# Performance work log

Hardware: AMD Instinct MI355X
Metric: run time of the kernel (lower is better)

The kernel has to match this reference:

```python
import jax, jax.numpy as jnp
import numpy as np

IMG = 224          # image_size
FMAP = (56, 56)    # feature_map_dims (AdaptiveAvgPool2d((56,56)))
K_REWEIGHT = 3     # self.n_reweight
BLUR_RADIUS = 4    # KNNGaussianBlur(4): kernel 9, sigma 4


def _cdist(a, b):
    # Euclidean pairwise distance, [Na, D] x [Nb, D] -> [Na, Nb]
    a2 = jnp.sum(a * a, axis=1, keepdims=True)            # [Na,1]
    b2 = jnp.sum(b * b, axis=1, keepdims=True).T          # [1,Nb]
    d2 = a2 + b2 - 2.0 * (a @ b.T)
    return jnp.sqrt(jnp.maximum(d2, 0.0))


def _gaussian_blur(x):
    # x: [1,1,H,W]; torchvision GaussianBlur(kernel=9, sigma=4), reflect pad
    r, sigma = BLUR_RADIUS, float(BLUR_RADIUS)
    t = jnp.arange(2 * r + 1, dtype=x.dtype) - r
    g = jnp.exp(-(t * t) / (2.0 * sigma * sigma))
    g = g / jnp.sum(g)
    k2d = jnp.outer(g, g)[None, None]                     # [1,1,9,9]
    xp = jnp.pad(x, ((0, 0), (0, 0), (r, r), (r, r)), mode='reflect')
    return jax.lax.conv_general_dilated(
        xp, k2d, window_strides=(1, 1), padding='VALID',
        dimension_numbers=('NCHW', 'OIHW', 'NCHW'))


def setup_inputs() -> dict:
    key = jax.random.key(0)
    k1, k2 = jax.random.split(key)
    patch = jax.random.normal(k1, (FMAP[0] * FMAP[1], 768), dtype=jnp.float32)
    patch_lib = jax.random.normal(k2, (16384, 768), dtype=jnp.float32)
    mean = jnp.zeros((), dtype=jnp.float32)
    std = jnp.ones((), dtype=jnp.float32)
    return {"patch": patch, "patch_lib": patch_lib, "mean": mean, "std": std}


def reference(patch, patch_lib, mean, std):
    # normalization (method_name != 'Point_MAE' branch)
    p = (patch - mean) / std                               # [N, D]

    dist = _cdist(p, patch_lib)                            # [N, Nlib]
    min_val = jnp.min(dist, axis=1)                        # [N]
    min_idx = jnp.argmin(dist, axis=1)                     # [N]
    s_idx = jnp.argmax(min_val)
    s_star = jnp.max(min_val)

    m_test = p[s_idx]                                      # [D]
    m_star = patch_lib[min_idx[s_idx]]                     # [D]

    # distances of m_star to whole bank, k smallest
    w_dist = jnp.sqrt(jnp.maximum(
        jnp.sum((patch_lib - m_star) ** 2, axis=1), 0.0))  # [Nlib]
    _, nn_idx = jax.lax.top_k(-w_dist, K_REWEIGHT)         # smallest k
    m_star_knn = jnp.linalg.norm(
        m_test[None, :] - patch_lib[nn_idx[1:]], axis=1)   # [k-1]

    D_sqrt = jnp.sqrt(jnp.asarray(patch.shape[1], dtype=p.dtype))
    w = 1.0 - jnp.exp(s_star / D_sqrt) / jnp.sum(jnp.exp(m_star_knn / D_sqrt))
    s = w * s_star

    s_map = min_val.reshape(1, 1, *FMAP)
    s_map = jax.image.resize(s_map, (1, 1, IMG, IMG), method='bilinear')
    s_map = _gaussian_blur(s_map)
    return s, s_map
```

## Files before the change

### kernel.cpp

```cpp
#include <hip/hip_runtime.h>
#include <hip/hip_bf16.h>
#include <stdint.h>

#define N_PATCH 3136
#define N_LIB   16384
#define DIM     768
#define IMGSZ   224
#define FM      56

#define BK 32
#define KT 24
#define NT 2
#define LDS_STRIDE 40
#define MT 25
#define NGRP 64

typedef __bf16 bf16_t;
typedef __bf16 bf16x8 __attribute__((ext_vector_type(8)));
typedef __bf16 bf16x4_v __attribute__((ext_vector_type(4)));
typedef float  f32x4  __attribute__((ext_vector_type(4)));

#define FLT_MAX_ 3.402823466e+38f

struct Scal {
  unsigned long long approx_max_pack;
  unsigned long long cand_pack[64];
  int cand[64];
  int cand_count;
  int s_idx;
  float s_star;
  int mstar_idx;
};

__device__ __forceinline__ float wave_reduce_sum(float v) {
#pragma unroll
  for (int s = 32; s > 0; s >>= 1) v += __shfl_xor(v, s, 64);
  return v;
}

__device__ __forceinline__ unsigned long long shfl_xor_u64(unsigned long long v, int mask) {
  unsigned lo = (unsigned)v, hi = (unsigned)(v >> 32);
  lo = __shfl_xor(lo, mask, 64);
  hi = __shfl_xor(hi, mask, 64);
  return ((unsigned long long)hi << 32) | lo;
}

__global__ void init_kernel(unsigned long long* __restrict__ minpack, Scal* sc) {
  int i = blockIdx.x * 256 + threadIdx.x;
  if (i < N_PATCH) minpack[i] = ~0ULL;
  if (i < 64) sc->cand_pack[i] = ~0ULL;
  if (i == 0) {
    sc->approx_max_pack = 0ULL;
    sc->cand_count = 0;
    sc->s_idx = 0; sc->s_star = 0.f; sc->mstar_idx = 0;
  }
}

__global__ void prep_patch_kernel(const float* __restrict__ patch,
                                  const float* __restrict__ meanp,
                                  const float* __restrict__ stdp,
                                  bf16_t* __restrict__ pb, float* __restrict__ a2) {
  __shared__ float sbuf[3];
  int row = blockIdx.x;
  int t = threadIdx.x;
  float mu = meanp[0], sd = stdp[0];
  float4 v = ((const float4*)(patch + (size_t)row * DIM))[t];
  v.x = (v.x - mu) / sd; v.y = (v.y - mu) / sd;
  v.z = (v.z - mu) / sd; v.w = (v.w - mu) / sd;
  bf16x4_v o = {(__bf16)v.x, (__bf16)v.y, (__bf16)v.z, (__bf16)v.w};
  *(bf16x4_v*)(pb + (size_t)row * DIM + t * 4) = o;
  float acc = v.x*v.x + v.y*v.y + v.z*v.z + v.w*v.w;
  acc = wave_reduce_sum(acc);
  if ((t & 63) == 0) sbuf[t >> 6] = acc;
  __syncthreads();
  if (t == 0) a2[row] = sbuf[0] + sbuf[1] + sbuf[2];
}

__global__ void prep_lib_kernel(const float* __restrict__ lib,
                                bf16_t* __restrict__ lb, float* __restrict__ b2) {
  __shared__ float sbuf[3];
  int row = blockIdx.x;
  int t = threadIdx.x;
  float4 v = ((const float4*)(lib + (size_t)row * DIM))[t];
  bf16x4_v o = {(__bf16)v.x, (__bf16)v.y, (__bf16)v.z, (__bf16)v.w};
  *(bf16x4_v*)(lb + (size_t)row * DIM + t * 4) = o;
  float acc = v.x*v.x + v.y*v.y + v.z*v.z + v.w*v.w;
  acc = wave_reduce_sum(acc);
  if ((t & 63) == 0) sbuf[t >> 6] = acc;
  __syncthreads();
  if (t == 0) b2[row] = sbuf[0] + sbuf[1] + sbuf[2];
}

__global__ __launch_bounds__(256, 2)
void gemm_min_kernel(const bf16_t* __restrict__ pb, const bf16_t* __restrict__ lb,
                     const float* __restrict__ a2, const float* __restrict__ b2,
                     unsigned long long* __restrict__ minpack) {
  __shared__ __align__(16) bf16_t As[2][128 * LDS_STRIDE];
  __shared__ __align__(16) bf16_t Bs[2][128 * LDS_STRIDE];

  const int t = threadIdx.x;
  const int wave = t >> 6;
  const int lane = t & 63;
  const int l15 = lane & 15;
  const int quad = lane >> 4;
  const int wm = (wave >> 1) * 64;
  const int wn = (wave & 1) * 64;

  const int lid = blockIdx.x;
  const int xcd = lid & 7;
  const int slot = lid >> 3;
  const int ygrp = xcd + 8 * (slot / MT);
  const int mtile = slot % MT;
  const int m0 = mtile * 128;
  const int n_base = ygrp * (NT * 128);

  const int srow = t >> 2;
  const int scol = (t & 3) * 8;

  int gr0 = m0 + srow;      if (gr0 > N_PATCH - 1) gr0 = N_PATCH - 1;
  int gr1 = m0 + srow + 64; if (gr1 > N_PATCH - 1) gr1 = N_PATCH - 1;
  const bf16_t* pA0 = pb + (size_t)gr0 * DIM + scol;
  const bf16_t* pA1 = pb + (size_t)gr1 * DIM + scol;
  const bf16_t* pB0 = lb + (size_t)(n_base + srow) * DIM + scol;
  const bf16_t* pB1 = pB0 + (size_t)64 * DIM;

  const int woff = srow * LDS_STRIDE + scol;

  {
    uint4 va0 = *(const uint4*)(pA0);
    uint4 va1 = *(const uint4*)(pA1);
    uint4 vb0 = *(const uint4*)(pB0);
    uint4 vb1 = *(const uint4*)(pB1);
    *(uint4*)(&As[0][woff]) = va0;
    *(uint4*)(&As[0][woff + 64 * LDS_STRIDE]) = va1;
    *(uint4*)(&Bs[0][woff]) = vb0;
    *(uint4*)(&Bs[0][woff + 64 * LDS_STRIDE]) = vb1;
  }
  __syncthreads();

  unsigned long long runmin[16];
#pragma unroll
  for (int i = 0; i < 16; i++) runmin[i] = ~0ULL;

  f32x4 acc[4][4];
#pragma unroll
  for (int mi = 0; mi < 4; mi++)
#pragma unroll
    for (int ni = 0; ni < 4; ni++) { f32x4 z = {0.f,0.f,0.f,0.f}; acc[mi][ni] = z; }

  int kt = 0, nt = 0;
  for (int i = 0; i < NT * KT; ++i) {
    const int cur = i & 1, nxt = cur ^ 1;
    int kt1 = kt + 1, nt1 = nt;
    if (kt1 == KT) { kt1 = 0; nt1++; }
    const bool hn = (nt1 < NT);

    uint4 va0, va1, vb0, vb1;
    if (hn) {
      size_t ka = (size_t)kt1 * BK;
      size_t kb = (size_t)nt1 * 128 * DIM + (size_t)kt1 * BK;
      va0 = *(const uint4*)(pA0 + ka);
      va1 = *(const uint4*)(pA1 + ka);
      vb0 = *(const uint4*)(pB0 + kb);
      vb1 = *(const uint4*)(pB1 + kb);
    }

    bf16x8 afr[4], bfr[4];
#pragma unroll
    for (int mi = 0; mi < 4; mi++)
      afr[mi] = *(const bf16x8*)(&As[cur][(wm + mi * 16 + l15) * LDS_STRIDE + quad * 8]);
#pragma unroll
    for (int ni = 0; ni < 4; ni++)
      bfr[ni] = *(const bf16x8*)(&Bs[cur][(wn + ni * 16 + l15) * LDS_STRIDE + quad * 8]);
#pragma unroll
    for (int mi = 0; mi < 4; mi++)
#pragma unroll
      for (int ni = 0; ni < 4; ni++)
        acc[mi][ni] = __builtin_amdgcn_mfma_f32_16x16x32_bf16(afr[mi], bfr[ni],
                                                              acc[mi][ni], 0, 0, 0);

    if (kt == KT - 1) {
      const int n0 = n_base + nt * 128;
      float b2n[4];
#pragma unroll
      for (int ni = 0; ni < 4; ni++) b2n[ni] = b2[n0 + wn + ni * 16 + l15];
#pragma unroll
      for (int mi = 0; mi < 4; mi++) {
#pragma unroll
        for (int r = 0; r < 4; r++) {
          int mrow = m0 + wm + mi * 16 + quad * 4 + r;
          float a2v = a2[mrow < N_PATCH ? mrow : (N_PATCH - 1)];
          unsigned long long best = ~0ULL;
#pragma unroll
          for (int ni = 0; ni < 4; ni++) {
            float d2v = a2v + b2n[ni] - 2.0f * acc[mi][ni][r];
            d2v = fmaxf(d2v, 0.0f);
            unsigned n = (unsigned)(n0 + wn + ni * 16 + l15);
            unsigned long long pk = (((unsigned long long)__float_as_uint(d2v)) << 32) | n;
            if (pk < best) best = pk;
          }
#pragma unroll
          for (int s = 1; s < 16; s <<= 1) {
            unsigned long long o = shfl_xor_u64(best, s);
            if (o < best) best = o;
          }
          if (best < runmin[mi * 4 + r]) runmin[mi * 4 + r] = best;
        }
      }
#pragma unroll
      for (int mi = 0; mi < 4; mi++)
#pragma unroll
        for (int ni = 0; ni < 4; ni++) { f32x4 z = {0.f,0.f,0.f,0.f}; acc[mi][ni] = z; }
    }

    if (hn) {
      *(uint4*)(&As[nxt][woff]) = va0;
      *(uint4*)(&As[nxt][woff + 64 * LDS_STRIDE]) = va1;
      *(uint4*)(&Bs[nxt][woff]) = vb0;
      *(uint4*)(&Bs[nxt][woff + 64 * LDS_STRIDE]) = vb1;
    }
    __syncthreads();
    kt = kt1; nt = nt1;
  }

  if (l15 == 0) {
#pragma unroll
    for (int mi = 0; mi < 4; mi++)
#pragma unroll
      for (int r = 0; r < 4; r++) {
        int mrow = m0 + wm + mi * 16 + quad * 4 + r;
        if (mrow < N_PATCH) atomicMin(&minpack[mrow], runmin[mi * 4 + r]);
      }
  }
}

__global__ void finalize_kernel(const unsigned long long* __restrict__ minpack,
                                float* __restrict__ min_val, int* __restrict__ min_idx,
                                Scal* sc) {
  int i = blockIdx.x * 256 + threadIdx.x;
  if (i >= N_PATCH) return;
  unsigned long long p = minpack[i];
  float d2 = __uint_as_float((unsigned)(p >> 32));
  float v = sqrtf(d2);
  min_val[i] = v;
  min_idx[i] = (int)(p & 0xffffffffu);
  unsigned long long mp = (((unsigned long long)__float_as_uint(v)) << 32) |
                          (unsigned)(0xffffffffu - (unsigned)i);
  atomicMax(&sc->approx_max_pack, mp);
}

__global__ void collect_kernel(const float* __restrict__ min_val, Scal* sc) {
  int i = blockIdx.x * 256 + threadIdx.x;
  if (i >= N_PATCH) return;
  float amax = __uint_as_float((unsigned)(sc->approx_max_pack >> 32));
  if (min_val[i] >= amax - 0.02f) {
    int p = atomicAdd(&sc->cand_count, 1);
    if (p < 64) sc->cand[p] = i;
  }
}

__global__ void refine_kernel(const float* __restrict__ patch, const float* __restrict__ lib,
                              const float* __restrict__ meanp, const float* __restrict__ stdp,
                              Scal* sc) {
  int c = blockIdx.x;
  int cnt = sc->cand_count; if (cnt > 64) cnt = 64;
  if (c >= cnt) return;
  int row = sc->cand[c];
  int wave = threadIdx.x >> 6, lane = threadIdx.x & 63;
  float mu = meanp[0], sd = stdp[0];
  float4 pv[3];
#pragma unroll
  for (int k = 0; k < 3; k++) {
    float4 v = ((const float4*)(patch + (size_t)row * DIM))[lane + 64 * k];
    v.x = (v.x - mu) / sd; v.y = (v.y - mu) / sd;
    v.z = (v.z - mu) / sd; v.w = (v.w - mu) / sd;
    pv[k] = v;
  }
  unsigned long long best = ~0ULL;
  int jbase = blockIdx.y * 128 + wave * 32;
  for (int rr = 0; rr < 32; rr++) {
    int j = jbase + rr;
    const float4* pl = (const float4*)(lib + (size_t)j * DIM);
    float acc = 0.f;
#pragma unroll
    for (int k = 0; k < 3; k++) {
      float4 l = pl[lane + 64 * k];
      float dx = pv[k].x - l.x, dy = pv[k].y - l.y;
      float dz = pv[k].z - l.z, dw = pv[k].w - l.w;
      acc += dx*dx + dy*dy + dz*dz + dw*dw;
    }
    acc = wave_reduce_sum(acc);
    unsigned long long pk = (((unsigned long long)__float_as_uint(acc)) << 32) | (unsigned)j;
    if (pk < best) best = pk;
  }
  if (lane == 0) atomicMin(&sc->cand_pack[c], best);
}

__global__ void pick_kernel(Scal* sc) {
  int lane = threadIdx.x;
  int cnt = sc->cand_count; if (cnt > 64) cnt = 64;
  unsigned long long pk = 0ULL;
  int row = 0, ms = 0;
  if (lane < cnt) {
    unsigned long long cp = sc->cand_pack[lane];
    row = sc->cand[lane];
    ms = (int)(cp & 0xffffffffu);
    unsigned d2b = (unsigned)(cp >> 32);
    pk = (((unsigned long long)d2b) << 32) | (unsigned)(0xffffffffu - (unsigned)row);
  }
  unsigned long long m = pk;
#pragma unroll
  for (int s = 1; s < 64; s <<= 1) {
    unsigned long long o = shfl_xor_u64(m, s);
    if (o > m) m = o;
  }
  if (lane < cnt && pk == m) {
    sc->s_idx = row;
    sc->s_star = sqrtf(__uint_as_float((unsigned)(m >> 32)));
    sc->mstar_idx = ms;
  }
}

__global__ void wdist_kernel(const float* __restrict__ lib, const Scal* __restrict__ sc,
                             float* __restrict__ wdist2) {
  int wave = threadIdx.x >> 6, lane = threadIdx.x & 63;
  int j = blockIdx.x * 4 + wave;
  int ms = sc->mstar_idx;
  const float4* pj = (const float4*)(lib + (size_t)j * DIM);
  const float4* pm = (const float4*)(lib + (size_t)ms * DIM);
  float acc = 0.f;
#pragma unroll
  for (int k = 0; k < 3; k++) {
    float4 a = pj[lane + 64 * k], b = pm[lane + 64 * k];
    float dx = a.x - b.x, dy = a.y - b.y, dz = a.z - b.z, dw = a.w - b.w;
    acc += dx*dx + dy*dy + dz*dz + dw*dw;
  }
  acc = wave_reduce_sum(acc);
  if (lane == 0) wdist2[j] = acc;
}

__global__ void top3_kernel(const float* __restrict__ wdist2,
                            const float* __restrict__ patch, const float* __restrict__ lib,
                            const float* __restrict__ meanp, const float* __restrict__ stdp,
                            const Scal* __restrict__ sc, float* __restrict__ out) {
  __shared__ unsigned long long sl[768];
  int t = threadIdx.x;

  unsigned long long b0 = ~0ULL, b1 = ~0ULL, b2 = ~0ULL;
  for (int j = t; j < N_LIB; j += 256) {
    unsigned long long pk = (((unsigned long long)__float_as_uint(wdist2[j])) << 32) | (unsigned)j;
    if (pk < b0)      { b2 = b1; b1 = b0; b0 = pk; }
    else if (pk < b1) { b2 = b1; b1 = pk; }
    else if (pk < b2) { b2 = pk; }
  }
  sl[t * 3 + 0] = b0; sl[t * 3 + 1] = b1; sl[t * 3 + 2] = b2;
  __syncthreads();
  if (t >= 64) return;

  unsigned long long c0 = ~0ULL, c1 = ~0ULL, c2 = ~0ULL;
#pragma unroll
  for (int e = 0; e < 12; e++) {
    unsigned long long pk = sl[t * 12 + e];
    if (pk < c0)      { c2 = c1; c1 = c0; c0 = pk; }
    else if (pk < c1) { c2 = c1; c1 = pk; }
    else if (pk < c2) { c2 = pk; }
  }
  unsigned long long res1 = 0, res2 = 0;
#pragma unroll
  for (int r = 0; r < 3; r++) {
    unsigned long long m = c0;
#pragma unroll
    for (int s = 1; s < 64; s <<= 1) {
      unsigned long long o = shfl_xor_u64(m, s);
      if (o < m) m = o;
    }
    if (r == 1) res1 = m;
    if (r == 2) res2 = m;
    if (c0 == m) { c0 = c1; c1 = c2; c2 = ~0ULL; }
  }
  int nA = (int)(res1 & 0xffffffffu);
  int nB = (int)(res2 & 0xffffffffu);

  int lane = t;
  int srow = sc->s_idx;
  float mu = meanp[0], sd = stdp[0];
  float accA = 0.f, accB = 0.f;
#pragma unroll
  for (int k = 0; k < 3; k++) {
    float4 p4 = ((const float4*)(patch + (size_t)srow * DIM))[lane + 64 * k];
    float4 a4 = ((const float4*)(lib + (size_t)nA * DIM))[lane + 64 * k];
    float4 b4 = ((const float4*)(lib + (size_t)nB * DIM))[lane + 64 * k];
    float px = (p4.x - mu) / sd, py = (p4.y - mu) / sd;
    float pz = (p4.z - mu) / sd, pw = (p4.w - mu) / sd;
    float dax = px - a4.x, day = py - a4.y, daz = pz - a4.z, daw = pw - a4.w;
    float dbx = px - b4.x, dby = py - b4.y, dbz = pz - b4.z, dbw = pw - b4.w;
    accA += dax*dax + day*day + daz*daz + daw*daw;
    accB += dbx*dbx + dby*dby + dbz*dbz + dbw*dbw;
  }
  accA = wave_reduce_sum(accA);
  accB = wave_reduce_sum(accB);
  if (lane == 0) {
    float dsq = sqrtf((float)DIM);
    float d1 = sqrtf(accA), d2v = sqrtf(accB);
    float sstar = sc->s_star;
    float w = 1.0f - expf(sstar / dsq) / (expf(d1 / dsq) + expf(d2v / dsq));
    out[0] = w * sstar;
  }
}

__global__ void resize_kernel(const float* __restrict__ mv, float* __restrict__ rz) {
  int o = blockIdx.x * 256 + threadIdx.x;
  if (o >= IMGSZ * IMGSZ) return;
  int y = o / IMGSZ, x = o % IMGSZ;
  float sy = 0.25f * y - 0.375f; sy = fminf(fmaxf(sy, 0.0f), 55.0f);
  float sx = 0.25f * x - 0.375f; sx = fminf(fmaxf(sx, 0.0f), 55.0f);
  int y0 = (int)sy; if (y0 > 54) y0 = 54;
  int x0 = (int)sx; if (x0 > 54) x0 = 54;
  float fy = sy - y0, fx = sx - x0;
  float v00 = mv[y0*FM + x0],     v01 = mv[y0*FM + x0 + 1];
  float v10 = mv[(y0+1)*FM + x0], v11 = mv[(y0+1)*FM + x0 + 1];
  float a = v00 + fx * (v01 - v00);
  float b = v10 + fx * (v11 - v10);
  rz[o] = a + fy * (b - a);
}

__global__ void blur_kernel(const float* __restrict__ rz, float* __restrict__ out) {
  int o = blockIdx.x * 256 + threadIdx.x;
  if (o >= IMGSZ * IMGSZ) return;
  int y = o / IMGSZ, x = o % IMGSZ;
  float g[9]; float gs = 0.f;
#pragma unroll
  for (int i = 0; i < 9; i++) { float tt = (float)(i - 4); g[i] = expf(-(tt*tt)/32.0f); gs += g[i]; }
#pragma unroll
  for (int i = 0; i < 9; i++) g[i] /= gs;
  float acc = 0.f;
#pragma unroll
  for (int dy = 0; dy < 9; dy++) {
    int yy = y + dy - 4;
    yy = yy < 0 ? -yy : (yy > IMGSZ - 1 ? 2*(IMGSZ-1) - yy : yy);
    float ra = 0.f;
#pragma unroll
    for (int dx = 0; dx < 9; dx++) {
      int xx = x + dx - 4;
      xx = xx < 0 ? -xx : (xx > IMGSZ - 1 ? 2*(IMGSZ-1) - xx : xx);
      ra += g[dx] * rz[yy*IMGSZ + xx];
    }
    acc += g[dy] * ra;
  }
  out[o] = acc;
}

extern "C" void kernel_launch(void* const* d_in, const int* in_sizes, int n_in,
                              void* d_out, int out_size, void* d_ws, size_t ws_size,
                              hipStream_t stream) {
  const float* patch = (const float*)d_in[0];
  const float* lib   = (const float*)d_in[1];
  const float* meanp = (const float*)d_in[2];
  const float* stdp  = (const float*)d_in[3];
  float* out = (float*)d_out;

  char* ws = (char*)d_ws;
  size_t off = 0;
  auto alloc = [&](size_t bytes) -> void* {
    void* p = ws + off;
    off = (off + bytes + 255) & ~(size_t)255;
    return p;
  };
  bf16_t* pb      = (bf16_t*)alloc((size_t)N_PATCH * DIM * sizeof(bf16_t));
  bf16_t* lb      = (bf16_t*)alloc((size_t)N_LIB * DIM * sizeof(bf16_t));
  float* a2       = (float*)alloc(N_PATCH * sizeof(float));
  float* b2       = (float*)alloc(N_LIB * sizeof(float));
  unsigned long long* minpack = (unsigned long long*)alloc(N_PATCH * 8);
  float* min_val  = (float*)alloc(N_PATCH * sizeof(float));
  int*   min_idx  = (int*)alloc(N_PATCH * sizeof(int));
  float* wdist2   = (float*)alloc(N_LIB * sizeof(float));
  float* resized  = (float*)alloc(IMGSZ * IMGSZ * sizeof(float));
  Scal*  sc       = (Scal*)alloc(sizeof(Scal));

  init_kernel<<<(N_PATCH + 255) / 256, 256, 0, stream>>>(minpack, sc);
  prep_patch_kernel<<<N_PATCH, 192, 0, stream>>>(patch, meanp, stdp, pb, a2);
  prep_lib_kernel<<<N_LIB, 192, 0, stream>>>(lib, lb, b2);
  gemm_min_kernel<<<MT * NGRP, 256, 0, stream>>>(pb, lb, a2, b2, minpack);
  finalize_kernel<<<(N_PATCH + 255) / 256, 256, 0, stream>>>(minpack, min_val, min_idx, sc);
  collect_kernel<<<(N_PATCH + 255) / 256, 256, 0, stream>>>(min_val, sc);
  refine_kernel<<<dim3(64, 128), 256, 0, stream>>>(patch, lib, meanp, stdp, sc);
  pick_kernel<<<1, 64, 0, stream>>>(sc);
  wdist_kernel<<<N_LIB / 4, 256, 0, stream>>>(lib, sc, wdist2);
  top3_kernel<<<1, 256, 0, stream>>>(wdist2, patch, lib, meanp, stdp, sc, out);
  resize_kernel<<<(IMGSZ * IMGSZ + 255) / 256, 256, 0, stream>>>(min_val, resized);
  blur_kernel<<<(IMGSZ * IMGSZ + 255) / 256, 256, 0, stream>>>(resized, out + 1);
}
```

Measured before the change: 368.8 us.

## Use direct global-to-LDS loads, one N tile per block, drop init/pick kernels

The GEMM-min kernel now loads tiles straight into LDS with global_load_lds, so the staging registers and the padded LDS stride go away. Each block now handles a single 128-column library tile and writes a per-tile float minimum to a partial buffer instead of doing 64-bit packed atomics. Finalize reduces those partials per row, and the separate init and pick kernels are folded into the prep and consumer kernels. Occupancy is raised to 3 blocks per SM and the prep kernels process one row per wave. The risks are LDS bank conflicts from the unpadded stride, and an extra write and read of the partial buffer.

```diff
diff --git a/kernel.cpp b/kernel.cpp
--- a/kernel.cpp
+++ b/kernel.cpp
@@ -3,6 +3,7 @@
 #include <stdint.h>
 
 #define N_PATCH 3136
+#define N_PATCH_PAD 3200
 #define N_LIB   16384
 #define DIM     768
 #define IMGSZ   224
@@ -10,10 +11,8 @@
 
 #define BK 32
 #define KT 24
-#define NT 2
-#define LDS_STRIDE 40
 #define MT 25
-#define NGRP 64
+#define NTILES 128
 
 typedef __bf16 bf16_t;
 typedef __bf16 bf16x8 __attribute__((ext_vector_type(8)));
@@ -27,9 +26,6 @@
   unsigned long long cand_pack[64];
   int cand[64];
   int cand_count;
-  int s_idx;
-  float s_star;
-  int mstar_idx;
 };
 
 __device__ __forceinline__ float wave_reduce_sum(float v) {
@@ -45,58 +41,63 @@
   return ((unsigned long long)hi << 32) | lo;
 }
 
-__global__ void init_kernel(unsigned long long* __restrict__ minpack, Scal* sc) {
-  int i = blockIdx.x * 256 + threadIdx.x;
-  if (i < N_PATCH) minpack[i] = ~0ULL;
-  if (i < 64) sc->cand_pack[i] = ~0ULL;
-  if (i == 0) {
-    sc->approx_max_pack = 0ULL;
-    sc->cand_count = 0;
-    sc->s_idx = 0; sc->s_star = 0.f; sc->mstar_idx = 0;
-  }
+__device__ __forceinline__ void async16(const bf16_t* g, bf16_t* l) {
+  __builtin_amdgcn_global_load_lds(
+      (const __attribute__((address_space(1))) unsigned int*)g,
+      (__attribute__((address_space(3))) unsigned int*)l, 16, 0, 0);
 }
 
 __global__ void prep_patch_kernel(const float* __restrict__ patch,
                                   const float* __restrict__ meanp,
                                   const float* __restrict__ stdp,
-                                  bf16_t* __restrict__ pb, float* __restrict__ a2) {
-  __shared__ float sbuf[3];
-  int row = blockIdx.x;
+                                  bf16_t* __restrict__ pb, float* __restrict__ a2,
+                                  Scal* sc) {
   int t = threadIdx.x;
+  int row = blockIdx.x * 4 + (t >> 6);
+  int lane = t & 63;
+  if (blockIdx.x == 0) {
+    if (t < 64) sc->cand_pack[t] = ~0ULL;
+    if (t == 0) { sc->approx_max_pack = 0ULL; sc->cand_count = 0; }
+  }
   float mu = meanp[0], sd = stdp[0];
-  float4 v = ((const float4*)(patch + (size_t)row * DIM))[t];
-  v.x = (v.x - mu) / sd; v.y = (v.y - mu) / sd;
-  v.z = (v.z - mu) / sd; v.w = (v.w - mu) / sd;
-  bf16x4_v o = {(__bf16)v.x, (__bf16)v.y, (__bf16)v.z, (__bf16)v.w};
-  *(bf16x4_v*)(pb + (size_t)row * DIM + t * 4) = o;
-  float acc = v.x*v.x + v.y*v.y + v.z*v.z + v.w*v.w;
+  float acc = 0.f;
+#pragma unroll
+  for (int k = 0; k < 3; k++) {
+    float4 v = ((const float4*)(patch + (size_t)row * DIM))[lane + 64 * k];
+    v.x = (v.x - mu) / sd; v.y = (v.y - mu) / sd;
+    v.z = (v.z - mu) / sd; v.w = (v.w - mu) / sd;
+    bf16x4_v o = {(__bf16)v.x, (__bf16)v.y, (__bf16)v.z, (__bf16)v.w};
+    *(bf16x4_v*)(pb + (size_t)row * DIM + (lane + 64 * k) * 4) = o;
+    acc += v.x*v.x + v.y*v.y + v.z*v.z + v.w*v.w;
+  }
   acc = wave_reduce_sum(acc);
-  if ((t & 63) == 0) sbuf[t >> 6] = acc;
-  __syncthreads();
-  if (t == 0) a2[row] = sbuf[0] + sbuf[1] + sbuf[2];
+  if (lane == 0) a2[row] = acc;
 }
 
 __global__ void prep_lib_kernel(const float* __restrict__ lib,
                                 bf16_t* __restrict__ lb, float* __restrict__ b2) {
-  __shared__ float sbuf[3];
-  int row = blockIdx.x;
   int t = threadIdx.x;
-  float4 v = ((const float4*)(lib + (size_t)row * DIM))[t];
-  bf16x4_v o = {(__bf16)v.x, (__bf16)v.y, (__bf16)v.z, (__bf16)v.w};
-  *(bf16x4_v*)(lb + (size_t)row * DIM + t * 4) = o;
-  float acc = v.x*v.x + v.y*v.y + v.z*v.z + v.w*v.w;
+  int row = blockIdx.x * 4 + (t >> 6);
+  int lane = t & 63;
+  float acc = 0.f;
+#pragma unroll
+  for (int k = 0; k < 3; k++) {
+    float4 v = ((const float4*)(lib + (size_t)row * DIM))[lane + 64 * k];
+    bf16x4_v o = {(__bf16)v.x, (__bf16)v.y, (__bf16)v.z, (__bf16)v.w};
+    *(bf16x4_v*)(lb + (size_t)row * DIM + (lane + 64 * k) * 4) = o;
+    acc += v.x*v.x + v.y*v.y + v.z*v.z + v.w*v.w;
+  }
   acc = wave_reduce_sum(acc);
-  if ((t & 63) == 0) sbuf[t >> 6] = acc;
-  __syncthreads();
-  if (t == 0) b2[row] = sbuf[0] + sbuf[1] + sbuf[2];
-}
-
-__global__ __launch_bounds__(256, 2)
+  if (lane == 0) b2[row] = acc;
+}
+
+__global__ __launch_bounds__(256, 3)
 void gemm_min_kernel(const bf16_t* __restrict__ pb, const bf16_t* __restrict__ lb,
                      const float* __restrict__ a2, const float* __restrict__ b2,
-                     unsigned long long* __restrict__ minpack) {
-  __shared__ __align__(16) bf16_t As[2][128 * LDS_STRIDE];
-  __shared__ __align__(16) bf16_t Bs[2][128 * LDS_STRIDE];
+                     float* __restrict__ part) {
+  __shared__ __align__(16) bf16_t As[2][128 * BK];
+  __shared__ __align__(16) bf16_t Bs[2][128 * BK];
+  __shared__ unsigned smin[128];
 
   const int t = threadIdx.x;
   const int wave = t >> 6;
@@ -109,144 +110,111 @@
   const int lid = blockIdx.x;
   const int xcd = lid & 7;
   const int slot = lid >> 3;
-  const int ygrp = xcd + 8 * (slot / MT);
+  const int ntile = xcd + 8 * (slot / MT);
   const int mtile = slot % MT;
   const int m0 = mtile * 128;
-  const int n_base = ygrp * (NT * 128);
-
-  const int srow = t >> 2;
-  const int scol = (t & 3) * 8;
-
-  int gr0 = m0 + srow;      if (gr0 > N_PATCH - 1) gr0 = N_PATCH - 1;
-  int gr1 = m0 + srow + 64; if (gr1 > N_PATCH - 1) gr1 = N_PATCH - 1;
-  const bf16_t* pA0 = pb + (size_t)gr0 * DIM + scol;
-  const bf16_t* pA1 = pb + (size_t)gr1 * DIM + scol;
-  const bf16_t* pB0 = lb + (size_t)(n_base + srow) * DIM + scol;
-  const bf16_t* pB1 = pB0 + (size_t)64 * DIM;
-
-  const int woff = srow * LDS_STRIDE + scol;
+  const int n0 = ntile * 128;
+
+  int ra0 = m0 + (t >> 2);       if (ra0 > N_PATCH - 1) ra0 = N_PATCH - 1;
+  int ra1 = m0 + 64 + (t >> 2);  if (ra1 > N_PATCH - 1) ra1 = N_PATCH - 1;
+  const bf16_t* gA0 = pb + (size_t)ra0 * DIM + (t & 3) * 8;
+  const bf16_t* gA1 = pb + (size_t)ra1 * DIM + (t & 3) * 8;
+  const bf16_t* gB0 = lb + (size_t)(n0 + (t >> 2)) * DIM + (t & 3) * 8;
+  const bf16_t* gB1 = gB0 + (size_t)64 * DIM;
+
+  if (t < 128) smin[t] = 0xffffffffu;
 
   {
-    uint4 va0 = *(const uint4*)(pA0);
-    uint4 va1 = *(const uint4*)(pA1);
-    uint4 vb0 = *(const uint4*)(pB0);
-    uint4 vb1 = *(const uint4*)(pB1);
-    *(uint4*)(&As[0][woff]) = va0;
-    *(uint4*)(&As[0][woff + 64 * LDS_STRIDE]) = va1;
-    *(uint4*)(&Bs[0][woff]) = vb0;
-    *(uint4*)(&Bs[0][woff + 64 * LDS_STRIDE]) = vb1;
+    bf16_t* la = &As[0][0];
+    bf16_t* lb_ = &Bs[0][0];
+    async16(gA0, la + t * 8);
+    async16(gA1, la + 2048 + t * 8);
+    async16(gB0, lb_ + t * 8);
+    async16(gB1, lb_ + 2048 + t * 8);
   }
   __syncthreads();
 
-  unsigned long long runmin[16];
-#pragma unroll
-  for (int i = 0; i < 16; i++) runmin[i] = ~0ULL;
-
   f32x4 acc[4][4];
 #pragma unroll
   for (int mi = 0; mi < 4; mi++)
 #pragma unroll
     for (int ni = 0; ni < 4; ni++) { f32x4 z = {0.f,0.f,0.f,0.f}; acc[mi][ni] = z; }
 
-  int kt = 0, nt = 0;
-  for (int i = 0; i < NT * KT; ++i) {
-    const int cur = i & 1, nxt = cur ^ 1;
-    int kt1 = kt + 1, nt1 = nt;
-    if (kt1 == KT) { kt1 = 0; nt1++; }
-    const bool hn = (nt1 < NT);
-
-    uint4 va0, va1, vb0, vb1;
-    if (hn) {
-      size_t ka = (size_t)kt1 * BK;
-      size_t kb = (size_t)nt1 * 128 * DIM + (size_t)kt1 * BK;
-      va0 = *(const uint4*)(pA0 + ka);
-      va1 = *(const uint4*)(pA1 + ka);
-      vb0 = *(const uint4*)(pB0 + kb);
-      vb1 = *(const uint4*)(pB1 + kb);
+  for (int k = 0; k < KT; ++k) {
+    const int cur = k & 1;
+    if (k + 1 < KT) {
+      const int nxt = cur ^ 1;
+      const size_t ko = (size_t)(k + 1) * BK;
+      bf16_t* la = &As[nxt][0];
+      bf16_t* lb_ = &Bs[nxt][0];
+      async16(gA0 + ko, la + t * 8);
+      async16(gA1 + ko, la + 2048 + t * 8);
+      async16(gB0 + ko, lb_ + t * 8);
+      async16(gB1 + ko, lb_ + 2048 + t * 8);
     }
 
     bf16x8 afr[4], bfr[4];
 #pragma unroll
     for (int mi = 0; mi < 4; mi++)
-      afr[mi] = *(const bf16x8*)(&As[cur][(wm + mi * 16 + l15) * LDS_STRIDE + quad * 8]);
+      afr[mi] = *(const bf16x8*)(&As[cur][(wm + mi * 16 + l15) * BK + quad * 8]);
 #pragma unroll
     for (int ni = 0; ni < 4; ni++)
-      bfr[ni] = *(const bf16x8*)(&Bs[cur][(wn + ni * 16 + l15) * LDS_STRIDE + quad * 8]);
+      bfr[ni] = *(const bf16x8*)(&Bs[cur][(wn + ni * 16 + l15) * BK + quad * 8]);
 #pragma unroll
     for (int mi = 0; mi < 4; mi++)
 #pragma unroll
       for (int ni = 0; ni < 4; ni++)
         acc[mi][ni] = __builtin_amdgcn_mfma_f32_16x16x32_bf16(afr[mi], bfr[ni],
                                                               acc[mi][ni], 0, 0, 0);
-
-    if (kt == KT - 1) {
-      const int n0 = n_base + nt * 128;
-      float b2n[4];
-#pragma unroll
-      for (int ni = 0; ni < 4; ni++) b2n[ni] = b2[n0 + wn + ni * 16 + l15];
-#pragma unroll
-      for (int mi = 0; mi < 4; mi++) {
-#pragma unroll
-        for (int r = 0; r < 4; r++) {
-          int mrow = m0 + wm + mi * 16 + quad * 4 + r;
-          float a2v = a2[mrow < N_PATCH ? mrow : (N_PATCH - 1)];
-          unsigned long long best = ~0ULL;
-#pragma unroll
-          for (int ni = 0; ni < 4; ni++) {
-            float d2v = a2v + b2n[ni] - 2.0f * acc[mi][ni][r];
-            d2v = fmaxf(d2v, 0.0f);
-            unsigned n = (unsigned)(n0 + wn + ni * 16 + l15);
-            unsigned long long pk = (((unsigned long long)__float_as_uint(d2v)) << 32) | n;
-            if (pk < best) best = pk;
-          }
-#pragma unroll
-          for (int s = 1; s < 16; s <<= 1) {
-            unsigned long long o = shfl_xor_u64(best, s);
-            if (o < best) best = o;
-          }
-          if (best < runmin[mi * 4 + r]) runmin[mi * 4 + r] = best;
-        }
-      }
-#pragma unroll
-      for (int mi = 0; mi < 4; mi++)
-#pragma unroll
-        for (int ni = 0; ni < 4; ni++) { f32x4 z = {0.f,0.f,0.f,0.f}; acc[mi][ni] = z; }
+    __syncthreads();
+  }
+
+  float b2n[4];
+#pragma unroll
+  for (int ni = 0; ni < 4; ni++) b2n[ni] = b2[n0 + wn + ni * 16 + l15];
+
+#pragma unroll
+  for (int mi = 0; mi < 4; mi++) {
+#pragma unroll
+    for (int r = 0; r < 4; r++) {
+      int rloc = wm + mi * 16 + quad * 4 + r;
+      int mrow = m0 + rloc;
+      float a2v = a2[mrow < N_PATCH ? mrow : (N_PATCH - 1)];
+      float best = a2v + b2n[0] - 2.0f * acc[mi][0][r];
+#pragma unroll
+      for (int ni = 1; ni < 4; ni++)
+        best = fminf(best, a2v + b2n[ni] - 2.0f * acc[mi][ni][r]);
+      best = fmaxf(best, 0.0f);
+#pragma unroll
+      for (int s = 1; s < 16; s <<= 1)
+        best = fminf(best, __shfl_xor(best, s, 64));
+      if (l15 == 0) atomicMin(&smin[rloc], __float_as_uint(best));
     }
-
-    if (hn) {
-      *(uint4*)(&As[nxt][woff]) = va0;
-      *(uint4*)(&As[nxt][woff + 64 * LDS_STRIDE]) = va1;
-      *(uint4*)(&Bs[nxt][woff]) = vb0;
-      *(uint4*)(&Bs[nxt][woff + 64 * LDS_STRIDE]) = vb1;
-    }
-    __syncthreads();
-    kt = kt1; nt = nt1;
-  }
-
-  if (l15 == 0) {
-#pragma unroll
-    for (int mi = 0; mi < 4; mi++)
-#pragma unroll
-      for (int r = 0; r < 4; r++) {
-        int mrow = m0 + wm + mi * 16 + quad * 4 + r;
-        if (mrow < N_PATCH) atomicMin(&minpack[mrow], runmin[mi * 4 + r]);
-      }
-  }
-}
-
-__global__ void finalize_kernel(const unsigned long long* __restrict__ minpack,
-                                float* __restrict__ min_val, int* __restrict__ min_idx,
-                                Scal* sc) {
-  int i = blockIdx.x * 256 + threadIdx.x;
-  if (i >= N_PATCH) return;
-  unsigned long long p = minpack[i];
-  float d2 = __uint_as_float((unsigned)(p >> 32));
-  float v = sqrtf(d2);
-  min_val[i] = v;
-  min_idx[i] = (int)(p & 0xffffffffu);
-  unsigned long long mp = (((unsigned long long)__float_as_uint(v)) << 32) |
-                          (unsigned)(0xffffffffu - (unsigned)i);
-  atomicMax(&sc->approx_max_pack, mp);
+  }
+  __syncthreads();
+  if (t < 128) part[(size_t)(m0 + t) * NTILES + ntile] = __uint_as_float(smin[t]);
+}
+
+__global__ void finalize_kernel(const float* __restrict__ part,
+                                float* __restrict__ min_val, Scal* sc) {
+  int t = threadIdx.x;
+  int row = blockIdx.x * 4 + (t >> 6);
+  int lane = t & 63;
+  if (row >= N_PATCH) return;
+  uint2 pv = *(const uint2*)(part + (size_t)row * NTILES + lane * 2);
+  unsigned m = pv.x < pv.y ? pv.x : pv.y;
+#pragma unroll
+  for (int s = 1; s < 64; s <<= 1) {
+    unsigned o = __shfl_xor((int)m, s, 64);
+    if (o < m) m = o;
+  }
+  if (lane == 0) {
+    float v = sqrtf(__uint_as_float(m));
+    min_val[row] = v;
+    unsigned long long mp = (((unsigned long long)__float_as_uint(v)) << 32) |
+                            (unsigned)(0xffffffffu - (unsigned)row);
+    atomicMax(&sc->approx_max_pack, mp);
+  }
 }
 
 __global__ void collect_kernel(const float* __restrict__ min_val, Scal* sc) {
@@ -296,17 +264,16 @@
   if (lane == 0) atomicMin(&sc->cand_pack[c], best);
 }
 
-__global__ void pick_kernel(Scal* sc) {
-  int lane = threadIdx.x;
+__device__ __forceinline__ void wave_pick(const Scal* sc, int lane,
+                                          int* srow, float* sstar, int* ms) {
   int cnt = sc->cand_count; if (cnt > 64) cnt = 64;
   unsigned long long pk = 0ULL;
-  int row = 0, ms = 0;
+  int rowv = 0, msv = 0;
   if (lane < cnt) {
     unsigned long long cp = sc->cand_pack[lane];
-    row = sc->cand[lane];
-    ms = (int)(cp & 0xffffffffu);
-    unsigned d2b = (unsigned)(cp >> 32);
-    pk = (((unsigned long long)d2b) << 32) | (unsigned)(0xffffffffu - (unsigned)row);
+    rowv = sc->cand[lane];
+    msv = (int)(cp & 0xffffffffu);
+    pk = (cp & 0xffffffff00000000ULL) | (unsigned)(0xffffffffu - (unsigned)rowv);
   }
   unsigned long long m = pk;
 #pragma unroll
@@ -314,18 +281,25 @@
     unsigned long long o = shfl_xor_u64(m, s);
     if (o > m) m = o;
   }
-  if (lane < cnt && pk == m) {
-    sc->s_idx = row;
-    sc->s_star = sqrtf(__uint_as_float((unsigned)(m >> 32)));
-    sc->mstar_idx = ms;
-  }
+  unsigned long long mask = __ballot(pk == m && lane < cnt);
+  int wl = (int)(__ffsll((long long)mask) - 1);
+  *srow = __shfl(rowv, wl, 64);
+  *ms   = __shfl(msv, wl, 64);
+  *sstar = sqrtf(__uint_as_float((unsigned)(m >> 32)));
 }
 
 __global__ void wdist_kernel(const float* __restrict__ lib, const Scal* __restrict__ sc,
                              float* __restrict__ wdist2) {
+  __shared__ int sms;
   int wave = threadIdx.x >> 6, lane = threadIdx.x & 63;
+  if (wave == 0) {
+    int srow, ms; float sstar;
+    wave_pick(sc, lane, &srow, &sstar, &ms);
+    if (lane == 0) sms = ms;
+  }
+  __syncthreads();
+  int ms = sms;
   int j = blockIdx.x * 4 + wave;
-  int ms = sc->mstar_idx;
   const float4* pj = (const float4*)(lib + (size_t)j * DIM);
   const float4* pm = (const float4*)(lib + (size_t)ms * DIM);
   float acc = 0.f;
@@ -381,15 +355,16 @@
   int nA = (int)(res1 & 0xffffffffu);
   int nB = (int)(res2 & 0xffffffffu);
 
-  int lane = t;
-  int srow = sc->s_idx;
+  int srow, ms; float sstar;
+  wave_pick(sc, t, &srow, &sstar, &ms);
+
   float mu = meanp[0], sd = stdp[0];
   float accA = 0.f, accB = 0.f;
 #pragma unroll
   for (int k = 0; k < 3; k++) {
-    float4 p4 = ((const float4*)(patch + (size_t)srow * DIM))[lane + 64 * k];
-    float4 a4 = ((const float4*)(lib + (size_t)nA * DIM))[lane + 64 * k];
-    float4 b4 = ((const float4*)(lib + (size_t)nB * DIM))[lane + 64 * k];
+    float4 p4 = ((const float4*)(patch + (size_t)srow * DIM))[t + 64 * k];
+    float4 a4 = ((const float4*)(lib + (size_t)nA * DIM))[t + 64 * k];
+    float4 b4 = ((const float4*)(lib + (size_t)nB * DIM))[t + 64 * k];
     float px = (p4.x - mu) / sd, py = (p4.y - mu) / sd;
     float pz = (p4.z - mu) / sd, pw = (p4.w - mu) / sd;
     float dax = px - a4.x, day = py - a4.y, daz = pz - a4.z, daw = pw - a4.w;
@@ -399,10 +374,9 @@
   }
   accA = wave_reduce_sum(accA);
   accB = wave_reduce_sum(accB);
-  if (lane == 0) {
+  if (t == 0) {
     float dsq = sqrtf((float)DIM);
     float d1 = sqrtf(accA), d2v = sqrtf(accB);
-    float sstar = sc->s_star;
     float w = 1.0f - expf(sstar / dsq) / (expf(d1 / dsq) + expf(d2v / dsq));
     out[0] = w * sstar;
   }
@@ -470,21 +444,18 @@
   bf16_t* lb      = (bf16_t*)alloc((size_t)N_LIB * DIM * sizeof(bf16_t));
   float* a2       = (float*)alloc(N_PATCH * sizeof(float));
   float* b2       = (float*)alloc(N_LIB * sizeof(float));
-  unsigned long long* minpack = (unsigned long long*)alloc(N_PATCH * 8);
+  float* part     = (float*)alloc((size_t)N_PATCH_PAD * NTILES * sizeof(float));
   float* min_val  = (float*)alloc(N_PATCH * sizeof(float));
-  int*   min_idx  = (int*)alloc(N_PATCH * sizeof(int));
   float* wdist2   = (float*)alloc(N_LIB * sizeof(float));
   float* resized  = (float*)alloc(IMGSZ * IMGSZ * sizeof(float));
   Scal*  sc       = (Scal*)alloc(sizeof(Scal));
 
-  init_kernel<<<(N_PATCH + 255) / 256, 256, 0, stream>>>(minpack, sc);
-  prep_patch_kernel<<<N_PATCH, 192, 0, stream>>>(patch, meanp, stdp, pb, a2);
-  prep_lib_kernel<<<N_LIB, 192, 0, stream>>>(lib, lb, b2);
-  gemm_min_kernel<<<MT * NGRP, 256, 0, stream>>>(pb, lb, a2, b2, minpack);
-  finalize_kernel<<<(N_PATCH + 255) / 256, 256, 0, stream>>>(minpack, min_val, min_idx, sc);
+  prep_patch_kernel<<<N_PATCH / 4, 256, 0, stream>>>(patch, meanp, stdp, pb, a2, sc);
+  prep_lib_kernel<<<N_LIB / 4, 256, 0, stream>>>(lib, lb, b2);
+  gemm_min_kernel<<<MT * NTILES, 256, 0, stream>>>(pb, lb, a2, b2, part);
+  finalize_kernel<<<N_PATCH / 4, 256, 0, stream>>>(part, min_val, sc);
   collect_kernel<<<(N_PATCH + 255) / 256, 256, 0, stream>>>(min_val, sc);
   refine_kernel<<<dim3(64, 128), 256, 0, stream>>>(patch, lib, meanp, stdp, sc);
-  pick_kernel<<<1, 64, 0, stream>>>(sc);
   wdist_kernel<<<N_LIB / 4, 256, 0, stream>>>(lib, sc, wdist2);
   top3_kernel<<<1, 256, 0, stream>>>(wdist2, patch, lib, meanp, stdp, sc, out);
   resize_kernel<<<(IMGSZ * IMGSZ + 255) / 256, 256, 0, stream>>>(min_val, resized);
```

Measured after the change: 374.1 us. Within noise of the previous version (+1.4%).
